# Performance work log

Measured on AMD Instinct MI355X. Metric: run time of the kernel, lower is better.

Reference implementation:

```python
import jax, jax.numpy as jnp
import numpy as np

B = 4
N1_PER = 16384  # fine points per scene
N2_PER = 4096   # coarse points per scene
IN_PLANES = 512
OUT_PLANES = 256
K = 3
CHUNK = 2048
BN_EPS = 1e-5


def _bn(x, g, b, m, v):
    # eval-mode BatchNorm1d: affine normalize with running stats
    return (x - m) * (g / jnp.sqrt(v + BN_EPS)) + b


def _interpolate_one(p1b, p2b, f2b):
    # p1b: [n1,3] queries, p2b: [n2,3] support, f2b: [n2,C]
    # k=3 inverse-distance weighted interpolation (pointops.interpolation)
    pq = p1b.reshape(-1, CHUNK, 3)  # chunk queries to avoid full [n1,n2] matrix

    def step(carry, q):  # q: [CHUNK,3]
        d2 = jnp.sum((q[:, None, :] - p2b[None, :, :]) ** 2, axis=-1)  # [CHUNK,n2]
        neg_d2, idx = jax.lax.top_k(-d2, K)                            # [CHUNK,K]
        dist = jnp.sqrt(jnp.maximum(-neg_d2, 1e-12))
        w = 1.0 / (dist + 1e-8)
        w = w / jnp.sum(w, axis=-1, keepdims=True)
        feat = f2b[idx]  # [CHUNK,K,C] gather
        return carry, jnp.einsum('qk,qkc->qc', w, feat)

    _, out = jax.lax.scan(step, None, pq)
    return out.reshape(-1, f2b.shape[-1])  # [n1,C]


def _forward(p1, x1, p2, x2, W1, b1, g1, be1, m1, v1, W2, b2, g2, be2, m2, v2):
    # branch 1: Linear-BN-ReLU on fine features
    h1 = jax.nn.relu(_bn(x1 @ W1.T + b1, g1, be1, m1, v1))  # [N1, out]
    # branch 2: Linear-BN-ReLU on coarse features, then kNN interpolation up
    h2 = jax.nn.relu(_bn(x2 @ W2.T + b2, g2, be2, m2, v2))  # [N2, out]
    # equal-sized scenes -> reshape + vmap over batch (offsets are [n,2n,...])
    p1b = p1.reshape(B, N1_PER, 3)
    p2b = p2.reshape(B, N2_PER, 3)
    h2b = h2.reshape(B, N2_PER, -1)
    up = jax.vmap(_interpolate_one)(p1b, p2b, h2b).reshape(-1, h2.shape[-1])
    return h1 + up


def setup_inputs() -> dict:
    key = jax.random.key(0)
    ks = jax.random.split(key, 16)
    p1 = jax.random.normal(ks[0], (B * N1_PER, 3), dtype=jnp.float32)
    x1 = jax.random.normal(ks[1], (B * N1_PER, OUT_PLANES), dtype=jnp.float32)
    p2 = jax.random.normal(ks[2], (B * N2_PER, 3), dtype=jnp.float32)
    x2 = jax.random.normal(ks[3], (B * N2_PER, IN_PLANES), dtype=jnp.float32)
    o1 = (jnp.arange(1, B + 1) * N1_PER).astype(jnp.int64)
    o2 = (jnp.arange(1, B + 1) * N2_PER).astype(jnp.int64)
    s1 = 1.0 / np.sqrt(OUT_PLANES)
    s2 = 1.0 / np.sqrt(IN_PLANES)
    W1 = jax.random.uniform(ks[4], (OUT_PLANES, OUT_PLANES), minval=-s1, maxval=s1)
    b1 = jax.random.uniform(ks[5], (OUT_PLANES,), minval=-s1, maxval=s1)
    W2 = jax.random.uniform(ks[6], (OUT_PLANES, IN_PLANES), minval=-s2, maxval=s2)
    b2 = jax.random.uniform(ks[7], (OUT_PLANES,), minval=-s2, maxval=s2)
    g1 = jnp.ones((OUT_PLANES,)); be1 = jnp.zeros((OUT_PLANES,))
    m1 = 0.1 * jax.random.normal(ks[8], (OUT_PLANES,))
    v1 = jax.random.uniform(ks[9], (OUT_PLANES,), minval=0.5, maxval=1.5)
    g2 = jnp.ones((OUT_PLANES,)); be2 = jnp.zeros((OUT_PLANES,))
    m2 = 0.1 * jax.random.normal(ks[10], (OUT_PLANES,))
    v2 = jax.random.uniform(ks[11], (OUT_PLANES,), minval=0.5, maxval=1.5)
    return dict(p1=p1, x1=x1, p2=p2, x2=x2, W1=W1, b1=b1, g1=g1, be1=be1,
                m1=m1, v1=v1, W2=W2, b2=b2, g2=g2, be2=be2, m2=m2, v2=v2,
                o1=o1, o2=o2)


def reference(p1, x1, p2, x2, W1, b1, g1, be1, m1, v1, W2, b2, g2, be2, m2, v2, o1, o2):
    return _forward(p1, x1, p2, x2, W1, b1, g1, be1, m1, v1, W2, b2, g2, be2, m2, v2)
```

## Files before the change

kernel.cpp:

```cpp
#include <hip/hip_runtime.h>

typedef __bf16 bf16x8 __attribute__((ext_vector_type(8)));
typedef float  f32x4  __attribute__((ext_vector_type(4)));
typedef float  f32x2  __attribute__((ext_vector_type(2)));

static __device__ __forceinline__ unsigned short f2bf(float f) {
  union { float f; unsigned int i; } c; c.f = f;
  unsigned int u = c.i;
  u += 0x7FFFu + ((u >> 16) & 1u);
  return (unsigned short)(u >> 16);
}

static __device__ __forceinline__ uint4 pk8(const float4 a, const float4 b) {
  uint4 o;
  o.x = ((unsigned int)f2bf(a.y) << 16) | f2bf(a.x);
  o.y = ((unsigned int)f2bf(a.w) << 16) | f2bf(a.z);
  o.z = ((unsigned int)f2bf(b.y) << 16) | f2bf(b.x);
  o.w = ((unsigned int)f2bf(b.w) << 16) | f2bf(b.z);
  return o;
}

static __device__ __forceinline__ bf16x8 pk8bf(const float4 a, const float4 b) {
  uint4 u = pk8(a, b);
  union { uint4 u; bf16x8 v; } c; c.u = u;
  return c.v;
}

#define WSEG0 65536u
#define WSEG1 196608u

__global__ __launch_bounds__(256) void cvt_w(const float* __restrict__ s0,
                                             const float* __restrict__ s1,
                                             unsigned short* __restrict__ dst) {
  const unsigned int e = (blockIdx.x * 256u + threadIdx.x) * 8u;
  const float* sp; unsigned int off;
  if (e < WSEG0) { sp = s0; off = e; }
  else           { sp = s1; off = e - WSEG0; }
  const float4* p = (const float4*)(sp + off);
  *(uint4*)(dst + e) = pk8(p[0], p[1]);
}

__global__ __launch_bounds__(256, 4) void gemm2_k(
    const float* __restrict__ A,
    const unsigned short* __restrict__ Wm,
    const float* __restrict__ bias,
    const float* __restrict__ gam,
    const float* __restrict__ bet,
    const float* __restrict__ rmean,
    const float* __restrict__ rvar,
    float* __restrict__ outp)
{
  constexpr int K   = 512;
  constexpr int KS  = 128;
  constexpr int LDW = KS + 8;
  __shared__ unsigned short WL[128][LDW];
  __shared__ float SC[128];
  __shared__ float SH[128];

  const int tid = threadIdx.x;
  const int bn = blockIdx.x;
  const int by = blockIdx.y;

  if (tid < 128) {
    const int ch = bn * 128 + tid;
    const float sc = gam[ch] / sqrtf(rvar[ch] + 1e-5f);
    SC[tid] = sc;
    SH[tid] = (bias[ch] - rmean[ch]) * sc + bet[ch];
  }

  const int wave = tid >> 6, lane = tid & 63;
  const int lr = lane & 15;
  const int kq = (lane >> 4) * 8;
  const int wrow0 = by * 64 + wave * 16;

  const float* Ap0 = A + (size_t)(wrow0 + lr) * K;

  f32x4 acc[8];
  const f32x4 zero = {0.f, 0.f, 0.f, 0.f};
#pragma unroll
  for (int ni = 0; ni < 8; ++ni) acc[ni] = zero;

  float4 aA[8], aB[8];

#define LOADA(buf, ph)                                                   \
  _Pragma("unroll")                                                      \
  for (int s = 0; s < 4; ++s) {                                          \
    buf[2*s]   = *(const float4*)(Ap0 + (ph)*KS + s*32 + kq);            \
    buf[2*s+1] = *(const float4*)(Ap0 + (ph)*KS + s*32 + kq + 4);        \
  }

#define STAGEW(ph)                                                       \
  _Pragma("unroll")                                                      \
  for (int i = tid; i < 128 * 16; i += 256) {                            \
    const int r = i >> 4, g = i & 15;                                    \
    *(uint4*)&WL[r][g*8] =                                               \
        *(const uint4*)(Wm + (size_t)(bn*128 + r)*K + (ph)*KS + g*8);    \
  }

#define COMPUTE(buf)                                                     \
  _Pragma("unroll")                                                      \
  for (int s = 0; s < 4; ++s) {                                          \
    const bf16x8 a0 = pk8bf(buf[2*s], buf[2*s+1]);                       \
    _Pragma("unroll")                                                    \
    for (int ni = 0; ni < 8; ++ni) {                                     \
      const bf16x8 bv = *(const bf16x8*)&WL[ni*16 + lr][s*32 + kq];      \
      acc[ni] = __builtin_amdgcn_mfma_f32_16x16x32_bf16(a0, bv, acc[ni], 0, 0, 0); \
    }                                                                    \
  }

  LOADA(aA, 0)
  STAGEW(0)
  LOADA(aB, 1)
  __syncthreads();
  COMPUTE(aA)
  __syncthreads();
  STAGEW(1)
  LOADA(aA, 2)
  __syncthreads();
  COMPUTE(aB)
  __syncthreads();
  STAGEW(2)
  LOADA(aB, 3)
  __syncthreads();
  COMPUTE(aA)
  __syncthreads();
  STAGEW(3)
  __syncthreads();
  COMPUTE(aB)

#undef LOADA
#undef STAGEW
#undef COMPUTE

#pragma unroll
  for (int r = 0; r < 4; ++r) {
    const int rloc = wave * 16 + (lane >> 4) * 4 + r;
    const size_t grow = (size_t)(by * 64 + rloc);
#pragma unroll
    for (int ni = 0; ni < 8; ++ni) {
      const int cloc = ni * 16 + lr;
      const int gcol = bn * 128 + cloc;
      float v = acc[ni][r] * SC[cloc] + SH[cloc];
      outp[grow * 256 + gcol] = fmaxf(v, 0.f);
    }
  }
}

__global__ __launch_bounds__(256, 3) void gemm_fused(
    const float* __restrict__ A,
    const unsigned short* __restrict__ Wm,
    const float* __restrict__ bias,
    const float* __restrict__ gam,
    const float* __restrict__ bet,
    const float* __restrict__ rmean,
    const float* __restrict__ rvar,
    float* __restrict__ outp,
    const float* __restrict__ h2f,
    const float* __restrict__ wgt,
    const int* __restrict__ idxg)
{
  constexpr int K   = 256;
  constexpr int KS  = 64;
  constexpr int LDW = KS + 8;
  constexpr int RPB = 64;
  __shared__ unsigned short WL[256][LDW];
  __shared__ float SC[256];
  __shared__ float SH[256];
  __shared__ float Wt[RPB * 3];
  __shared__ int   Id[RPB * 3];

  const int tid = threadIdx.x;
  const int by = blockIdx.x;

  {
    const int ch = tid;
    const float sc = gam[ch] / sqrtf(rvar[ch] + 1e-5f);
    SC[ch] = sc;
    SH[ch] = (bias[ch] - rmean[ch]) * sc + bet[ch];
  }
  if (tid < RPB * 3) {
    Wt[tid] = wgt[by * (RPB * 3) + tid];
    Id[tid] = idxg[by * (RPB * 3) + tid];
  }

  const int wave = tid >> 6, lane = tid & 63;
  const int lr = lane & 15;
  const int kq = (lane >> 4) * 8;
  const int wrow0 = by * RPB + wave * 16;

  const float* Ap0 = A + (size_t)(wrow0 + lr) * K;

  f32x4 acc[16];
  const f32x4 zero = {0.f, 0.f, 0.f, 0.f};
#pragma unroll
  for (int ni = 0; ni < 16; ++ni) acc[ni] = zero;

  float4 aA[4], aB[4];

#define LOADA(buf, ph)                                                   \
  buf[0] = *(const float4*)(Ap0 + (ph)*KS + kq);                         \
  buf[1] = *(const float4*)(Ap0 + (ph)*KS + kq + 4);                     \
  buf[2] = *(const float4*)(Ap0 + (ph)*KS + 32 + kq);                    \
  buf[3] = *(const float4*)(Ap0 + (ph)*KS + 32 + kq + 4);

#define STAGEW(ph)                                                       \
  _Pragma("unroll")                                                      \
  for (int i = tid; i < 256 * 8; i += 256) {                             \
    const int r = i >> 3, g = i & 7;                                     \
    *(uint4*)&WL[r][g*8] =                                               \
        *(const uint4*)(Wm + (size_t)r * K + (ph)*KS + g*8);             \
  }

#define COMPUTE(buf)                                                     \
  _Pragma("unroll")                                                      \
  for (int s = 0; s < 2; ++s) {                                          \
    const bf16x8 a0 = pk8bf(buf[2*s], buf[2*s+1]);                       \
    _Pragma("unroll")                                                    \
    for (int ni = 0; ni < 16; ++ni) {                                    \
      const bf16x8 bv = *(const bf16x8*)&WL[ni*16 + lr][s*32 + kq];      \
      acc[ni] = __builtin_amdgcn_mfma_f32_16x16x32_bf16(a0, bv, acc[ni], 0, 0, 0); \
    }                                                                    \
  }

  LOADA(aA, 0)
  STAGEW(0)
  LOADA(aB, 1)
  __syncthreads();
  COMPUTE(aA)
  __syncthreads();
  STAGEW(1)
  LOADA(aA, 2)
  __syncthreads();
  COMPUTE(aB)
  __syncthreads();
  STAGEW(2)
  LOADA(aB, 3)
  __syncthreads();
  COMPUTE(aA)
  __syncthreads();
  STAGEW(3)
  __syncthreads();
  COMPUTE(aB)

#undef LOADA
#undef STAGEW
#undef COMPUTE

#pragma unroll
  for (int r = 0; r < 4; ++r) {
    const int rloc = wave * 16 + (lane >> 4) * 4 + r;
    const size_t grow = (size_t)(by * RPB + rloc);
    const float w0 = Wt[rloc * 3 + 0], w1 = Wt[rloc * 3 + 1], w2 = Wt[rloc * 3 + 2];
    const float* g0 = h2f + (size_t)Id[rloc * 3 + 0] * 256;
    const float* g1 = h2f + (size_t)Id[rloc * 3 + 1] * 256;
    const float* g2 = h2f + (size_t)Id[rloc * 3 + 2] * 256;
#pragma unroll
    for (int ni = 0; ni < 16; ++ni) {
      const int gcol = ni * 16 + lr;
      float v = acc[ni][r] * SC[gcol] + SH[gcol];
      v = fmaxf(v, 0.f);
      v += w0 * g0[gcol] + w1 * g1[gcol] + w2 * g2[gcol];
      outp[grow * 256 + gcol] = v;
    }
  }
}

__global__ __launch_bounds__(256) void prep_pairs(const float* __restrict__ p2,
                                                  float* __restrict__ pp) {
  const int m = blockIdx.x * 256 + threadIdx.x;
  const float* s = p2 + m * 6;
  float* d = pp + m * 8;
  d[0] = s[0]; d[1] = s[3];
  d[2] = s[1]; d[3] = s[4];
  d[4] = s[2]; d[5] = s[5];
  d[6] = 0.f;  d[7] = 0.f;
}

__global__ __launch_bounds__(256) void knn_partial(const float* __restrict__ p1,
                                                   const float* __restrict__ ppair,
                                                   float* __restrict__ s_part,
                                                   int* __restrict__ i_part) {
#pragma clang fp contract(off)
  const int tid = threadIdx.x;
  const int qb = blockIdx.x, sp = blockIdx.y;
  const int scene = qb >> 6;
  const int pbase = scene * 4096 + sp * 512;
  const int qi = qb * 256 + tid;

  const float qx = p1[qi * 3 + 0];
  const float qy = p1[qi * 3 + 1];
  const float qz = p1[qi * 3 + 2];
  const f32x2 qxx = {qx, qx}, qyy = {qy, qy}, qzz = {qz, qz};

  float s0 = 1e30f, s1 = 1e30f, s2 = 1e30f;
  int i0 = pbase, i1 = pbase, i2 = pbase;

  const f32x2* pp = (const f32x2*)(ppair + (size_t)(pbase >> 1) * 8);
#pragma unroll 4
  for (int m = 0; m < 256; ++m) {
    const f32x2 X = pp[m * 4 + 0];
    const f32x2 Y = pp[m * 4 + 1];
    const f32x2 Z = pp[m * 4 + 2];
    const f32x2 dx = qxx - X;
    const f32x2 dy = qyy - Y;
    const f32x2 dz = qzz - Z;
    const f32x2 sv = (dx * dx + dy * dy) + dz * dz;
    const int jg = pbase + 2 * m;
    const float sa = sv.x, sb = sv.y;
    if (sa < s2) {
      if (sa < s1) {
        s2 = s1; i2 = i1;
        if (sa < s0) { s1 = s0; i1 = i0; s0 = sa; i0 = jg; }
        else         { s1 = sa; i1 = jg; }
      } else { s2 = sa; i2 = jg; }
    }
    if (sb < s2) {
      if (sb < s1) {
        s2 = s1; i2 = i1;
        if (sb < s0) { s1 = s0; i1 = i0; s0 = sb; i0 = jg + 1; }
        else         { s1 = sb; i1 = jg + 1; }
      } else { s2 = sb; i2 = jg + 1; }
    }
  }
  const int ob = (qi * 8 + sp) * 3;
  s_part[ob + 0] = s0; s_part[ob + 1] = s1; s_part[ob + 2] = s2;
  i_part[ob + 0] = i0; i_part[ob + 1] = i1; i_part[ob + 2] = i2;
}

__global__ __launch_bounds__(256) void knn_merge(const float* __restrict__ s_part,
                                                 const int* __restrict__ i_part,
                                                 float* __restrict__ wgt,
                                                 int* __restrict__ idxg) {
  const int qi = blockIdx.x * 256 + threadIdx.x;

  float s0 = 1e30f, s1 = 1e30f, s2 = 1e30f;
  int i0 = 0, i1 = 0, i2 = 0;
  const int base = qi * 24;
#pragma unroll
  for (int t = 0; t < 24; ++t) {
    const float s = s_part[base + t];
    const int id = i_part[base + t];
    if (s < s2) {
      if (s < s1) {
        s2 = s1; i2 = i1;
        if (s < s0) { s1 = s0; i1 = i0; s0 = s; i0 = id; }
        else        { s1 = s;  i1 = id; }
      } else { s2 = s; i2 = id; }
    }
  }
  const float d0 = sqrtf(fmaxf(s0, 1e-12f));
  const float d1 = sqrtf(fmaxf(s1, 1e-12f));
  const float d2 = sqrtf(fmaxf(s2, 1e-12f));
  float w0 = 1.f / (d0 + 1e-8f);
  float w1 = 1.f / (d1 + 1e-8f);
  float w2 = 1.f / (d2 + 1e-8f);
  const float inv = 1.f / (w0 + w1 + w2);
  wgt[qi * 3 + 0] = w0 * inv; wgt[qi * 3 + 1] = w1 * inv; wgt[qi * 3 + 2] = w2 * inv;
  idxg[qi * 3 + 0] = i0; idxg[qi * 3 + 1] = i1; idxg[qi * 3 + 2] = i2;
}

extern "C" void kernel_launch(void* const* d_in, const int* in_sizes, int n_in,
                              void* d_out, int out_size, void* d_ws, size_t ws_size,
                              hipStream_t stream) {
  const float* p1 = (const float*)d_in[0];
  const float* x1 = (const float*)d_in[1];
  const float* p2 = (const float*)d_in[2];
  const float* x2 = (const float*)d_in[3];
  const float* W1 = (const float*)d_in[4];
  const float* b1 = (const float*)d_in[5];
  const float* g1 = (const float*)d_in[6];
  const float* be1 = (const float*)d_in[7];
  const float* m1 = (const float*)d_in[8];
  const float* v1 = (const float*)d_in[9];
  const float* W2 = (const float*)d_in[10];
  const float* b2 = (const float*)d_in[11];
  const float* g2 = (const float*)d_in[12];
  const float* be2 = (const float*)d_in[13];
  const float* m2 = (const float*)d_in[14];
  const float* v2 = (const float*)d_in[15];

  char* ws = (char*)d_ws;
  unsigned short* W1b = (unsigned short*)ws;
  unsigned short* W2b = (unsigned short*)(ws + 131072);
  float* s_part = (float*)(ws + 1048576);
  int*   i_part = (int*)(ws + 7340032);
  float* h2f    = (float*)(ws + 16777216);
  float* ppair  = (float*)(ws + 33554432);
  float* wgt    = (float*)(ws + 33816576);
  int*   idxg   = (int*)(ws + 34603008);

  float* outp = (float*)d_out;

  cvt_w<<<96, 256, 0, stream>>>(W1, W2, W1b);

  gemm2_k<<<dim3(2, 256), 256, 0, stream>>>(
      x2, W2b, b2, g2, be2, m2, v2, h2f);

  prep_pairs<<<32, 256, 0, stream>>>(p2, ppair);

  knn_partial<<<dim3(256, 8), 256, 0, stream>>>(p1, ppair, s_part, i_part);

  knn_merge<<<256, 256, 0, stream>>>(s_part, i_part, wgt, idxg);

  gemm_fused<<<1024, 256, 0, stream>>>(
      x1, W1b, b1, g1, be1, m1, v1, outp, h2f, wgt, idxg);
}
```

Measured before the change: 338.5 us.

## Swizzle GEMM block order across XCDs and make kNN top-3 insertion branchless

```diff
diff --git a/kernel.cpp b/kernel.cpp
--- a/kernel.cpp
+++ b/kernel.cpp
@@ -170,7 +170,9 @@
   __shared__ int   Id[RPB * 3];
 
   const int tid = threadIdx.x;
-  const int by = blockIdx.x;
+  const int d = blockIdx.x;
+  const int xcd = d & 7, slot = d >> 3;
+  const int by = ((xcd >> 1) << 8) | (slot << 1) | (xcd & 1);
 
   {
     const int ch = tid;
@@ -296,7 +298,7 @@
   int i0 = pbase, i1 = pbase, i2 = pbase;
 
   const f32x2* pp = (const f32x2*)(ppair + (size_t)(pbase >> 1) * 8);
-#pragma unroll 4
+#pragma unroll 8
   for (int m = 0; m < 256; ++m) {
     const f32x2 X = pp[m * 4 + 0];
     const f32x2 Y = pp[m * 4 + 1];
@@ -307,19 +309,27 @@
     const f32x2 sv = (dx * dx + dy * dy) + dz * dz;
     const int jg = pbase + 2 * m;
     const float sa = sv.x, sb = sv.y;
-    if (sa < s2) {
-      if (sa < s1) {
-        s2 = s1; i2 = i1;
-        if (sa < s0) { s1 = s0; i1 = i0; s0 = sa; i0 = jg; }
-        else         { s1 = sa; i1 = jg; }
-      } else { s2 = sa; i2 = jg; }
-    }
-    if (sb < s2) {
-      if (sb < s1) {
-        s2 = s1; i2 = i1;
-        if (sb < s0) { s1 = s0; i1 = i0; s0 = sb; i0 = jg + 1; }
-        else         { s1 = sb; i1 = jg + 1; }
-      } else { s2 = sb; i2 = jg + 1; }
+    if (fminf(sa, sb) < s2) {
+      {
+        const bool c2 = sa < s2, c1 = sa < s1, c0 = sa < s0;
+        const float ns2 = c1 ? s1 : (c2 ? sa : s2);
+        const int   nj2 = c1 ? i1 : (c2 ? jg : i2);
+        const float ns1 = c0 ? s0 : (c1 ? sa : s1);
+        const int   nj1 = c0 ? i0 : (c1 ? jg : i1);
+        s0 = c0 ? sa : s0; i0 = c0 ? jg : i0;
+        s1 = ns1; i1 = nj1;
+        s2 = ns2; i2 = nj2;
+      }
+      {
+        const bool c2 = sb < s2, c1 = sb < s1, c0 = sb < s0;
+        const float ns2 = c1 ? s1 : (c2 ? sb : s2);
+        const int   nj2 = c1 ? i1 : (c2 ? (jg + 1) : i2);
+        const float ns1 = c0 ? s0 : (c1 ? sb : s1);
+        const int   nj1 = c0 ? i0 : (c1 ? (jg + 1) : i1);
+        s0 = c0 ? sb : s0; i0 = c0 ? (jg + 1) : i0;
+        s1 = ns1; i1 = nj1;
+        s2 = ns2; i2 = nj2;
+      }
     }
   }
   const int ob = (qi * 8 + sp) * 3;
```

Result: slower. 359.5 us (+6.2%).
